# Kernel optimization log

Hardware: AMD Instinct MI355X
Metric: run time of the kernel (lower is better)

## Reference

```python
import jax, jax.numpy as jnp
import numpy as np

B, S, DIM = 2, 2048, 1024
HID = 2048          # multiple_of-rounded hidden dim
E, NSH, TOPK = 8, 2, 2


def _ffn(x, w1, w2, w3):
    return (jax.nn.silu(x @ w1.T) * (x @ w3.T)) @ w2.T


def setup_inputs() -> dict:
    key = jax.random.key(0)
    ks = jax.random.split(key, 8)
    sc = 0.02  # init scale for stability
    return {
        "x": jax.random.normal(ks[0], (B, S, DIM), jnp.float32),
        "router_w": jax.random.normal(ks[1], (E, DIM), jnp.float32) * sc,
        "expert_bias": jnp.zeros((E,), jnp.float32),
        "w1": jax.random.normal(ks[2], (E, HID, DIM), jnp.float32) * sc,
        "w3": jax.random.normal(ks[3], (E, HID, DIM), jnp.float32) * sc,
        "w2": jax.random.normal(ks[4], (E, DIM, HID), jnp.float32) * sc,
        "sw1": jax.random.normal(ks[5], (NSH, HID, DIM), jnp.float32) * sc,
        "sw3": jax.random.normal(ks[6], (NSH, HID, DIM), jnp.float32) * sc,
        "sw2": jax.random.normal(ks[7], (NSH, DIM, HID), jnp.float32) * sc,
    }


def reference(x, router_w, expert_bias, w1, w3, w2, sw1, sw3, sw2):
    bs, sl, d = x.shape
    xf = x.reshape(-1, d)  # [T, d]

    # shared experts (always-on)
    shared = jnp.zeros_like(xf)
    for i in range(sw1.shape[0]):
        shared = shared + _ffn(xf, sw1[i], sw2[i], sw3[i])

    # router with aux-free load-balance bias
    logits = xf @ router_w.T + expert_bias  # [T, E]
    rw, sel = jax.lax.top_k(logits, TOPK)   # [T, K]
    rw = jax.nn.softmax(rw.astype(jnp.float32), axis=-1).astype(x.dtype)

    # combine weights per (token, expert): sum of routing weights over topk slots
    onehot = jax.nn.one_hot(sel, E, dtype=x.dtype)        # [T, K, E]
    combine = jnp.einsum('tk,tke->te', rw, onehot)        # [T, E]

    # per-expert FFN accumulated via scan (equivalent to gather-FFN-scatter)
    def body(acc, ew):
        e1, e3, e2, cw = ew  # cw: [T]
        acc = acc + cw[:, None] * _ffn(xf, e1, e2, e3)
        return acc, None

    out, _ = jax.lax.scan(body, jnp.zeros_like(xf), (w1, w3, w2, combine.T))
    out = out + shared
    return out.reshape(bs, sl, -1)
```

## Files before the change

### kernel.cpp

```cpp
#include <hip/hip_runtime.h>
#include <stdint.h>

#define T_TOK 4096
#define DIMD  1024
#define HIDN  2048
#define NEXP  8
#define RMAX  9216
#define RROWS (RMAX + 2 * T_TOK)

typedef float f32x4 __attribute__((ext_vector_type(4)));
typedef short s16x8 __attribute__((ext_vector_type(8)));

__device__ __forceinline__ uint16_t f2bf(float f) {
    uint32_t u = __builtin_bit_cast(uint32_t, f);
    u += 0x7fffu + ((u >> 16) & 1u);
    return (uint16_t)(u >> 16);
}
__device__ __forceinline__ float bf2f(uint32_t h) {
    return __builtin_bit_cast(float, h << 16);
}
__device__ __forceinline__ uint32_t pk2(float a, float b) {
    return (uint32_t)f2bf(a) | ((uint32_t)f2bf(b) << 16);
}
__device__ __forceinline__ int swz(int r, int cbyte) {
    return r * 128 + (cbyte ^ ((r & 7) << 4));
}
__device__ __forceinline__ void gload16(const void* g, void* l) {
    __builtin_amdgcn_global_load_lds(
        (const __attribute__((address_space(1))) void*)g,
        (__attribute__((address_space(3))) void*)l, 16, 0, 0);
}
__device__ __forceinline__ void stage128x64(const uint16_t* gbase, int ldk,
                                            char* lds, int wv, int lane) {
    #pragma unroll
    for (int i = 0; i < 4; ++i) {
        int s = (wv * 4 + i) * 64 + lane;
        int row = s >> 3;
        int cb = ((s & 7) << 4) ^ ((row & 7) << 4);
        gload16(gbase + (size_t)row * ldk + (cb >> 1), lds + ((wv * 4 + i) << 10));
    }
}


struct CvtArgs {
    const float* s[7];
    uint16_t*    d[7];
    int          ng[7];
};

__global__ void cvt_all_kernel(CvtArgs a) {
    int base = blockIdx.x * blockDim.x + threadIdx.x;
    int stride = gridDim.x * blockDim.x;
    #pragma unroll
    for (int seg = 0; seg < 7; ++seg) {
        const float4* sp = (const float4*)a.s[seg];
        uint4* dp = (uint4*)a.d[seg];
        int n = a.ng[seg];
        for (int i = base; i < n; i += stride) {
            float4 v0 = sp[2 * i];
            float4 v1 = sp[2 * i + 1];
            uint4 o;
            o.x = pk2(v0.x, v0.y); o.y = pk2(v0.z, v0.w);
            o.z = pk2(v1.x, v1.y); o.w = pk2(v1.z, v1.w);
            dp[i] = o;
        }
    }
}

__global__ __launch_bounds__(256)
void router_kernel(const float* __restrict__ x, const float* __restrict__ rw,
                   const float* __restrict__ bias,
                   int* __restrict__ sel, float* __restrict__ wgt,
                   int* __restrict__ cnt) {
    __shared__ float rws[NEXP * DIMD];
    int tid = threadIdx.x;
    for (int i = tid; i < NEXP * DIMD / 4; i += 256)
        ((float4*)rws)[i] = ((const float4*)rw)[i];
    __syncthreads();

    int wid = tid >> 6, lane = tid & 63;
    float b[NEXP];
    #pragma unroll
    for (int e = 0; e < NEXP; ++e) b[e] = bias[e];

    int t0 = (blockIdx.x * 4 + wid) * 8;
    for (int j = 0; j < 8; ++j) {
        int t = t0 + j;
        const float4* xr = (const float4*)(x + (size_t)t * DIMD);
        float p[NEXP] = {};
        #pragma unroll
        for (int c = 0; c < 4; ++c) {
            float4 xv = xr[c * 64 + lane];
            #pragma unroll
            for (int e = 0; e < NEXP; ++e) {
                float4 wv = *(const float4*)(rws + e * DIMD + c * 256 + lane * 4);
                p[e] += xv.x * wv.x + xv.y * wv.y + xv.z * wv.z + xv.w * wv.w;
            }
        }
        #pragma unroll
        for (int off = 32; off >= 1; off >>= 1) {
            #pragma unroll
            for (int e = 0; e < NEXP; ++e) p[e] += __shfl_xor(p[e], off, 64);
        }
        if (lane == 0) {
            #pragma unroll
            for (int e = 0; e < NEXP; ++e) p[e] += b[e];
            float l0 = -1e30f; int i0 = 0;
            #pragma unroll
            for (int e = 0; e < NEXP; ++e) { if (p[e] > l0) { l0 = p[e]; i0 = e; } }
            float l1 = -1e30f; int i1 = 0;
            #pragma unroll
            for (int e = 0; e < NEXP; ++e) { if (e == i0) continue; if (p[e] > l1) { l1 = p[e]; i1 = e; } }
            float e1 = expf(l1 - l0);
            float d = 1.f + e1;
            sel[t * 2] = i0; sel[t * 2 + 1] = i1;
            wgt[t * 2] = 1.f / d; wgt[t * 2 + 1] = e1 / d;
            atomicAdd(&cnt[i0], 1);
            atomicAdd(&cnt[i1], 1);
        }
    }
}

__global__ void offs_kernel(const int* __restrict__ cnt, int* __restrict__ offs) {
    if (threadIdx.x == 0 && blockIdx.x == 0) {
        int o = 0;
        for (int e = 0; e < NEXP; ++e) { offs[e] = o; o += (cnt[e] + 127) & ~127; }
        offs[NEXP] = o;
    }
}

__global__ void assign_kernel(const int* __restrict__ sel, const int* __restrict__ offs,
                              int* __restrict__ fill, int* __restrict__ row_of,
                              int* __restrict__ tok) {
    int i = blockIdx.x * blockDim.x + threadIdx.x;
    if (i < 2 * T_TOK) {
        int e = sel[i];
        int r = offs[e] + atomicAdd(&fill[e], 1);
        row_of[i] = r;
        tok[r] = i >> 1;
    } else if (i < 4 * T_TOK) {
        int j = i - 2 * T_TOK;
        tok[offs[NEXP] + j] = j & (T_TOK - 1);
    }
}

__global__ void combine_kernel(const uint16_t* __restrict__ H2, const int* __restrict__ row_of,
                               const float* __restrict__ wgt, const int* __restrict__ offs,
                               float* __restrict__ out) {
    int t = blockIdx.x;
    int c = threadIdx.x * 8;
    int r0 = row_of[t * 2], r1 = row_of[t * 2 + 1];
    int s0 = offs[NEXP] + t, s1 = s0 + T_TOK;
    float w0 = wgt[t * 2], w1 = wgt[t * 2 + 1];
    uint4 a = *(const uint4*)(H2 + (size_t)r0 * DIMD + c);
    uint4 b = *(const uint4*)(H2 + (size_t)r1 * DIMD + c);
    uint4 u = *(const uint4*)(H2 + (size_t)s0 * DIMD + c);
    uint4 v = *(const uint4*)(H2 + (size_t)s1 * DIMD + c);
    float4 o0, o1;
    o0.x = w0 * bf2f(a.x & 0xffffu) + w1 * bf2f(b.x & 0xffffu) + bf2f(u.x & 0xffffu) + bf2f(v.x & 0xffffu);
    o0.y = w0 * bf2f(a.x >> 16)     + w1 * bf2f(b.x >> 16)     + bf2f(u.x >> 16)     + bf2f(v.x >> 16);
    o0.z = w0 * bf2f(a.y & 0xffffu) + w1 * bf2f(b.y & 0xffffu) + bf2f(u.y & 0xffffu) + bf2f(v.y & 0xffffu);
    o0.w = w0 * bf2f(a.y >> 16)     + w1 * bf2f(b.y >> 16)     + bf2f(u.y >> 16)     + bf2f(v.y >> 16);
    o1.x = w0 * bf2f(a.z & 0xffffu) + w1 * bf2f(b.z & 0xffffu) + bf2f(u.z & 0xffffu) + bf2f(v.z & 0xffffu);
    o1.y = w0 * bf2f(a.z >> 16)     + w1 * bf2f(b.z >> 16)     + bf2f(u.z >> 16)     + bf2f(v.z >> 16);
    o1.z = w0 * bf2f(a.w & 0xffffu) + w1 * bf2f(b.w & 0xffffu) + bf2f(u.w & 0xffffu) + bf2f(v.w & 0xffffu);
    o1.w = w0 * bf2f(a.w >> 16)     + w1 * bf2f(b.w >> 16)     + bf2f(u.w >> 16)     + bf2f(v.w >> 16);
    float* o = out + (size_t)t * DIMD + c;
    *(float4*)o = o0;
    *(float4*)(o + 4) = o1;
}


__global__ __launch_bounds__(256, 2)
void gemm13_kernel(const uint16_t* __restrict__ xb, const int* __restrict__ tok,
                   const uint16_t* __restrict__ W1, const uint16_t* __restrict__ W3,
                   uint16_t* __restrict__ H, const int* __restrict__ offs) {
    __shared__ __align__(16) char lds[49152];
    char* As  = lds;
    char* B1s = lds + 16384;
    char* B3s = lds + 32768;

    const int K = DIMD;
    int row0 = blockIdx.y * 128;
    int rsh = row0 - offs[NEXP];
    int e;
    if (rsh >= 0) {
        if (rsh >= 2 * T_TOK) return;
        e = NEXP + (rsh >> 12);
    } else {
        e = 0;
        while (row0 >= offs[e + 1]) ++e;
    }
    const uint16_t* b1 = W1 + (size_t)e * HIDN * DIMD;
    const uint16_t* b3 = W3 + (size_t)e * HIDN * DIMD;
    int col0 = blockIdx.x * 128;

    int tid = threadIdx.x, lane = tid & 63;
    int wv = tid >> 6, wm = wv >> 1, wn = wv & 1;

    size_t abase[4];
    #pragma unroll
    for (int i = 0; i < 4; ++i) {
        int s = (wv * 4 + i) * 64 + lane;
        int row = s >> 3;
        int cb = ((s & 7) << 4) ^ ((row & 7) << 4);
        abase[i] = (size_t)tok[row0 + row] * DIMD + (cb >> 1);
    }

    f32x4 acc1[4][4] = {};
    f32x4 acc3[4][4] = {};

    for (int kt = 0; kt < K; kt += 64) {
        __syncthreads();
        #pragma unroll
        for (int i = 0; i < 4; ++i)
            gload16(xb + abase[i] + kt, As + ((wv * 4 + i) << 10));
        stage128x64(b1 + (size_t)col0 * K + kt, K, B1s, wv, lane);
        stage128x64(b3 + (size_t)col0 * K + kt, K, B3s, wv, lane);
        __syncthreads();

        #pragma unroll
        for (int s = 0; s < 2; ++s) {
            int cb = s * 64 + ((lane >> 4) << 4);
            s16x8 av[4];
            #pragma unroll
            for (int i = 0; i < 4; ++i)
                av[i] = *(const s16x8*)(As + swz(wm * 64 + i * 16 + (lane & 15), cb));
            #pragma unroll
            for (int j = 0; j < 4; ++j) {
                int br = wn * 64 + j * 16 + (lane & 15);
                s16x8 bv1 = *(const s16x8*)(B1s + swz(br, cb));
                s16x8 bv3 = *(const s16x8*)(B3s + swz(br, cb));
                #pragma unroll
                for (int i = 0; i < 4; ++i) {
                    acc1[i][j] = __builtin_amdgcn_mfma_f32_16x16x32_bf16(av[i], bv1, acc1[i][j], 0, 0, 0);
                    acc3[i][j] = __builtin_amdgcn_mfma_f32_16x16x32_bf16(av[i], bv3, acc3[i][j], 0, 0, 0);
                }
            }
        }
    }

    #pragma unroll
    for (int i = 0; i < 4; ++i) {
        #pragma unroll
        for (int j = 0; j < 4; ++j) {
            #pragma unroll
            for (int rg = 0; rg < 4; ++rg) {
                int row = row0 + wm * 64 + i * 16 + ((lane >> 4) << 2) + rg;
                int col = col0 + wn * 64 + j * 16 + (lane & 15);
                float a1 = acc1[i][j][rg];
                float a3 = acc3[i][j][rg];
                float hv = (a1 / (1.f + __expf(-a1))) * a3;
                H[(size_t)row * HIDN + col] = f2bf(hv);
            }
        }
    }
}

__global__ __launch_bounds__(256, 3)
void gemm2_kernel(const uint16_t* __restrict__ Hg,
                  const uint16_t* __restrict__ W2, uint16_t* __restrict__ H2,
                  const int* __restrict__ offs) {
    __shared__ __align__(16) char lds[32768];
    char* As = lds;
    char* Bs = lds + 16384;

    const int K = HIDN;
    int row0 = blockIdx.y * 128;
    int rsh = row0 - offs[NEXP];
    int e;
    if (rsh >= 0) {
        if (rsh >= 2 * T_TOK) return;
        e = NEXP + (rsh >> 12);
    } else {
        e = 0;
        while (row0 >= offs[e + 1]) ++e;
    }
    const uint16_t* b2 = W2 + (size_t)e * DIMD * HIDN;
    int col0 = blockIdx.x * 128;

    int tid = threadIdx.x, lane = tid & 63;
    int wv = tid >> 6, wm = wv >> 1, wn = wv & 1;

    f32x4 acc[4][4] = {};

    for (int kt = 0; kt < K; kt += 64) {
        __syncthreads();
        stage128x64(Hg + (size_t)row0 * K + kt, K, As, wv, lane);
        stage128x64(b2 + (size_t)col0 * K + kt, K, Bs, wv, lane);
        __syncthreads();

        #pragma unroll
        for (int s = 0; s < 2; ++s) {
            int cb = s * 64 + ((lane >> 4) << 4);
            s16x8 av[4];
            #pragma unroll
            for (int i = 0; i < 4; ++i)
                av[i] = *(const s16x8*)(As + swz(wm * 64 + i * 16 + (lane & 15), cb));
            #pragma unroll
            for (int j = 0; j < 4; ++j) {
                s16x8 bv = *(const s16x8*)(Bs + swz(wn * 64 + j * 16 + (lane & 15), cb));
                #pragma unroll
                for (int i = 0; i < 4; ++i)
                    acc[i][j] = __builtin_amdgcn_mfma_f32_16x16x32_bf16(av[i], bv, acc[i][j], 0, 0, 0);
            }
        }
    }

    #pragma unroll
    for (int i = 0; i < 4; ++i) {
        #pragma unroll
        for (int j = 0; j < 4; ++j) {
            #pragma unroll
            for (int rg = 0; rg < 4; ++rg) {
                int row = row0 + wm * 64 + i * 16 + ((lane >> 4) << 2) + rg;
                int col = col0 + wn * 64 + j * 16 + (lane & 15);
                H2[(size_t)row * DIMD + col] = f2bf(acc[i][j][rg]);
            }
        }
    }
}


extern "C" void kernel_launch(void* const* d_in, const int* in_sizes, int n_in,
                              void* d_out, int out_size, void* d_ws, size_t ws_size,
                              hipStream_t stream) {
    const float* x   = (const float*)d_in[0];
    const float* rw  = (const float*)d_in[1];
    const float* eb  = (const float*)d_in[2];
    const float* w1  = (const float*)d_in[3];
    const float* w3  = (const float*)d_in[4];
    const float* w2  = (const float*)d_in[5];
    const float* sw1 = (const float*)d_in[6];
    const float* sw3 = (const float*)d_in[7];
    const float* sw2 = (const float*)d_in[8];
    float* out = (float*)d_out;

    const size_t EW = (size_t)NEXP * HIDN * DIMD;
    const size_t SW = (size_t)2 * HIDN * DIMD;

    char* ws = (char*)d_ws;
    size_t off = 0;
    auto alloc = [&](size_t b) { char* p = ws + off; off = (off + b + 255) & ~(size_t)255; return p; };
    uint16_t* xb    = (uint16_t*)alloc((size_t)T_TOK * DIMD * 2);
    uint16_t* Hg    = (uint16_t*)alloc((size_t)RROWS * HIDN * 2);
    uint16_t* H2    = (uint16_t*)alloc((size_t)RROWS * DIMD * 2);
    uint16_t* w1all = (uint16_t*)alloc((EW + SW) * 2);
    uint16_t* w3all = (uint16_t*)alloc((EW + SW) * 2);
    uint16_t* w2all = (uint16_t*)alloc((EW + SW) * 2);
    int*   sel    = (int*)  alloc(T_TOK * 2 * 4);
    float* wgt    = (float*)alloc(T_TOK * 2 * 4);
    int*   row_of = (int*)  alloc(T_TOK * 2 * 4);
    int*   tok    = (int*)  alloc(RROWS * 4);
    int*   cntfill= (int*)  alloc(128);
    int*   offs   = (int*)  alloc(64);
    int*   cnt  = cntfill;
    int*   fill = cntfill + 16;

    hipMemsetAsync(cntfill, 0, 128, stream);
    hipMemsetAsync(tok, 0, RROWS * 4, stream);

    CvtArgs ca;
    ca.s[0] = w1;  ca.d[0] = w1all;      ca.ng[0] = (int)(EW / 8);
    ca.s[1] = sw1; ca.d[1] = w1all + EW; ca.ng[1] = (int)(SW / 8);
    ca.s[2] = w3;  ca.d[2] = w3all;      ca.ng[2] = (int)(EW / 8);
    ca.s[3] = sw3; ca.d[3] = w3all + EW; ca.ng[3] = (int)(SW / 8);
    ca.s[4] = w2;  ca.d[4] = w2all;      ca.ng[4] = (int)(EW / 8);
    ca.s[5] = sw2; ca.d[5] = w2all + EW; ca.ng[5] = (int)(SW / 8);
    ca.s[6] = x;   ca.d[6] = xb;         ca.ng[6] = T_TOK * DIMD / 8;
    cvt_all_kernel<<<2048, 256, 0, stream>>>(ca);

    router_kernel<<<128, 256, 0, stream>>>(x, rw, eb, sel, wgt, cnt);
    offs_kernel<<<1, 1, 0, stream>>>(cnt, offs);
    assign_kernel<<<64, 256, 0, stream>>>(sel, offs, fill, row_of, tok);

    gemm13_kernel<<<dim3(HIDN / 128, RROWS / 128), 256, 0, stream>>>(xb, tok, w1all, w3all, Hg, offs);
    gemm2_kernel<<<dim3(DIMD / 128, RROWS / 128), 256, 0, stream>>>(Hg, w2all, H2, offs);

    combine_kernel<<<T_TOK, 128, 0, stream>>>(H2, row_of, wgt, offs, out);
}
```

Before: 477.4 us.

## Fuse x bf16 conversion into router and widen gemm2 tiles to 256 rows

The fp32-to-bf16 conversion of x moves out of the bulk convert kernel and into the router kernel, which already reads x, so x is read only once. gemm2 now gives each block 256 rows as two 128-row sub-tiles, each with its own expert weight, and each wave computes a 128x64 sub-tile with 8x4 accumulators. This halves the grid in the row dimension and uses 64KB of LDS with occupancy 2. The block loads B tiles for two experts when they differ, so B reuse only improves when both halves share an expert, and the extra registers may reduce occupancy.

```diff
diff --git a/kernel.cpp b/kernel.cpp
--- a/kernel.cpp
+++ b/kernel.cpp
@@ -43,16 +43,16 @@
 
 
 struct CvtArgs {
-    const float* s[7];
-    uint16_t*    d[7];
-    int          ng[7];
+    const float* s[6];
+    uint16_t*    d[6];
+    int          ng[6];
 };
 
 __global__ void cvt_all_kernel(CvtArgs a) {
     int base = blockIdx.x * blockDim.x + threadIdx.x;
     int stride = gridDim.x * blockDim.x;
     #pragma unroll
-    for (int seg = 0; seg < 7; ++seg) {
+    for (int seg = 0; seg < 6; ++seg) {
         const float4* sp = (const float4*)a.s[seg];
         uint4* dp = (uint4*)a.d[seg];
         int n = a.ng[seg];
@@ -71,7 +71,7 @@
 void router_kernel(const float* __restrict__ x, const float* __restrict__ rw,
                    const float* __restrict__ bias,
                    int* __restrict__ sel, float* __restrict__ wgt,
-                   int* __restrict__ cnt) {
+                   int* __restrict__ cnt, uint16_t* __restrict__ xb) {
     __shared__ float rws[NEXP * DIMD];
     int tid = threadIdx.x;
     for (int i = tid; i < NEXP * DIMD / 4; i += 256)
@@ -91,6 +91,8 @@
         #pragma unroll
         for (int c = 0; c < 4; ++c) {
             float4 xv = xr[c * 64 + lane];
+            uint2 o; o.x = pk2(xv.x, xv.y); o.y = pk2(xv.z, xv.w);
+            *(uint2*)(xb + (size_t)t * DIMD + c * 256 + lane * 4) = o;
             #pragma unroll
             for (int e = 0; e < NEXP; ++e) {
                 float4 wv = *(const float4*)(rws + e * DIMD + c * 256 + lane * 4);
@@ -171,6 +173,14 @@
 }
 
 
+__device__ __forceinline__ int expert_of(int row, const int* offs) {
+    int rsh = row - offs[NEXP];
+    if (rsh >= 0) return (rsh < 2 * T_TOK) ? (NEXP + (rsh >> 12)) : NEXP;
+    int e = 0;
+    while (row >= offs[e + 1]) ++e;
+    return e;
+}
+
 __global__ __launch_bounds__(256, 2)
 void gemm13_kernel(const uint16_t* __restrict__ xb, const int* __restrict__ tok,
                    const uint16_t* __restrict__ W1, const uint16_t* __restrict__ W3,
@@ -182,15 +192,8 @@
 
     const int K = DIMD;
     int row0 = blockIdx.y * 128;
-    int rsh = row0 - offs[NEXP];
-    int e;
-    if (rsh >= 0) {
-        if (rsh >= 2 * T_TOK) return;
-        e = NEXP + (rsh >> 12);
-    } else {
-        e = 0;
-        while (row0 >= offs[e + 1]) ++e;
-    }
+    if (row0 - offs[NEXP] >= 2 * T_TOK) return;
+    int e = expert_of(row0, offs);
     const uint16_t* b1 = W1 + (size_t)e * HIDN * DIMD;
     const uint16_t* b3 = W3 + (size_t)e * HIDN * DIMD;
     int col0 = blockIdx.x * 128;
@@ -257,63 +260,64 @@
     }
 }
 
-__global__ __launch_bounds__(256, 3)
+__global__ __launch_bounds__(256, 2)
 void gemm2_kernel(const uint16_t* __restrict__ Hg,
                   const uint16_t* __restrict__ W2, uint16_t* __restrict__ H2,
                   const int* __restrict__ offs) {
-    __shared__ __align__(16) char lds[32768];
-    char* As = lds;
-    char* Bs = lds + 16384;
+    __shared__ __align__(16) char lds[65536];
+    char* As0 = lds;
+    char* As1 = lds + 16384;
+    char* Bs0 = lds + 32768;
+    char* Bs1 = lds + 49152;
 
     const int K = HIDN;
-    int row0 = blockIdx.y * 128;
-    int rsh = row0 - offs[NEXP];
-    int e;
-    if (rsh >= 0) {
-        if (rsh >= 2 * T_TOK) return;
-        e = NEXP + (rsh >> 12);
-    } else {
-        e = 0;
-        while (row0 >= offs[e + 1]) ++e;
-    }
-    const uint16_t* b2 = W2 + (size_t)e * DIMD * HIDN;
+    int row0 = blockIdx.y * 256;
+    if (row0 - offs[NEXP] >= 2 * T_TOK) return;
+    int e0 = expert_of(row0, offs);
+    int e1 = expert_of(row0 + 128, offs);
+    const uint16_t* b20 = W2 + (size_t)e0 * DIMD * HIDN;
+    const uint16_t* b21 = W2 + (size_t)e1 * DIMD * HIDN;
     int col0 = blockIdx.x * 128;
 
     int tid = threadIdx.x, lane = tid & 63;
     int wv = tid >> 6, wm = wv >> 1, wn = wv & 1;
 
-    f32x4 acc[4][4] = {};
+    f32x4 acc[8][4] = {};
 
     for (int kt = 0; kt < K; kt += 64) {
         __syncthreads();
-        stage128x64(Hg + (size_t)row0 * K + kt, K, As, wv, lane);
-        stage128x64(b2 + (size_t)col0 * K + kt, K, Bs, wv, lane);
+        stage128x64(Hg + (size_t)row0 * K + kt, K, As0, wv, lane);
+        stage128x64(Hg + (size_t)(row0 + 128) * K + kt, K, As1, wv, lane);
+        stage128x64(b20 + (size_t)col0 * K + kt, K, Bs0, wv, lane);
+        stage128x64(b21 + (size_t)col0 * K + kt, K, Bs1, wv, lane);
         __syncthreads();
 
+        char* As = wm ? As1 : As0;
+        char* Bs = wm ? Bs1 : Bs0;
         #pragma unroll
         for (int s = 0; s < 2; ++s) {
             int cb = s * 64 + ((lane >> 4) << 4);
-            s16x8 av[4];
-            #pragma unroll
-            for (int i = 0; i < 4; ++i)
-                av[i] = *(const s16x8*)(As + swz(wm * 64 + i * 16 + (lane & 15), cb));
-            #pragma unroll
-            for (int j = 0; j < 4; ++j) {
-                s16x8 bv = *(const s16x8*)(Bs + swz(wn * 64 + j * 16 + (lane & 15), cb));
+            s16x8 bv[4];
+            #pragma unroll
+            for (int j = 0; j < 4; ++j)
+                bv[j] = *(const s16x8*)(Bs + swz(wn * 64 + j * 16 + (lane & 15), cb));
+            #pragma unroll
+            for (int i = 0; i < 8; ++i) {
+                s16x8 av = *(const s16x8*)(As + swz(i * 16 + (lane & 15), cb));
                 #pragma unroll
-                for (int i = 0; i < 4; ++i)
-                    acc[i][j] = __builtin_amdgcn_mfma_f32_16x16x32_bf16(av[i], bv, acc[i][j], 0, 0, 0);
-            }
-        }
-    }
-
-    #pragma unroll
-    for (int i = 0; i < 4; ++i) {
+                for (int j = 0; j < 4; ++j)
+                    acc[i][j] = __builtin_amdgcn_mfma_f32_16x16x32_bf16(av, bv[j], acc[i][j], 0, 0, 0);
+            }
+        }
+    }
+
+    #pragma unroll
+    for (int i = 0; i < 8; ++i) {
         #pragma unroll
         for (int j = 0; j < 4; ++j) {
             #pragma unroll
             for (int rg = 0; rg < 4; ++rg) {
-                int row = row0 + wm * 64 + i * 16 + ((lane >> 4) << 2) + rg;
+                int row = row0 + wm * 128 + i * 16 + ((lane >> 4) << 2) + rg;
                 int col = col0 + wn * 64 + j * 16 + (lane & 15);
                 H2[(size_t)row * DIMD + col] = f2bf(acc[i][j][rg]);
             }
@@ -367,15 +371,14 @@
     ca.s[3] = sw3; ca.d[3] = w3all + EW; ca.ng[3] = (int)(SW / 8);
     ca.s[4] = w2;  ca.d[4] = w2all;      ca.ng[4] = (int)(EW / 8);
     ca.s[5] = sw2; ca.d[5] = w2all + EW; ca.ng[5] = (int)(SW / 8);
-    ca.s[6] = x;   ca.d[6] = xb;         ca.ng[6] = T_TOK * DIMD / 8;
     cvt_all_kernel<<<2048, 256, 0, stream>>>(ca);
 
-    router_kernel<<<128, 256, 0, stream>>>(x, rw, eb, sel, wgt, cnt);
+    router_kernel<<<128, 256, 0, stream>>>(x, rw, eb, sel, wgt, cnt, xb);
     offs_kernel<<<1, 1, 0, stream>>>(cnt, offs);
     assign_kernel<<<64, 256, 0, stream>>>(sel, offs, fill, row_of, tok);
 
     gemm13_kernel<<<dim3(HIDN / 128, RROWS / 128), 256, 0, stream>>>(xb, tok, w1all, w3all, Hg, offs);
-    gemm2_kernel<<<dim3(DIMD / 128, RROWS / 128), 256, 0, stream>>>(Hg, w2all, H2, offs);
+    gemm2_kernel<<<dim3(DIMD / 128, RROWS / 256), 256, 0, stream>>>(Hg, w2all, H2, offs);
 
     combine_kernel<<<T_TOK, 128, 0, stream>>>(H2, row_of, wgt, offs, out);
 }
```

New measurement: 501.6 us. +5.1%, slower.
